# Kernel tuning notes

Measured on AMD Instinct MI355X. Metric: run time of the kernel, lower is better.

The kernel has to match this reference:

```python
import jax, jax.numpy as jnp
import numpy as np

N = 50000      # nodes
E = 800000     # edges (avg degree 16)
IN_DIM = 128
HIDDEN = 128
HEADS = 4
OUT = HIDDEN // HEADS  # 32 per-head out dim
NEG_SLOPE = 0.2        # DGL GATConv default leaky_relu slope


def setup_inputs() -> dict:
    key = jax.random.key(0)
    ks = jax.random.split(key, 12)
    x = jax.random.normal(ks[0], (N, IN_DIM), dtype=jnp.float32)
    src = jax.random.randint(ks[1], (E,), 0, N)
    dst = jax.random.randint(ks[2], (E,), 0, N)
    s = 0.1
    # layer 1 params
    W1 = jax.random.normal(ks[3], (IN_DIM, HEADS * OUT), dtype=jnp.float32) * s
    al1 = jax.random.normal(ks[4], (HEADS, OUT), dtype=jnp.float32) * s
    ar1 = jax.random.normal(ks[5], (HEADS, OUT), dtype=jnp.float32) * s
    b1 = jnp.zeros((HEADS * OUT,), dtype=jnp.float32)
    # layer 2 params (input = flattened heads of layer 1 = HIDDEN)
    W2 = jax.random.normal(ks[6], (HIDDEN, HEADS * OUT), dtype=jnp.float32) * s
    al2 = jax.random.normal(ks[7], (HEADS, OUT), dtype=jnp.float32) * s
    ar2 = jax.random.normal(ks[8], (HEADS, OUT), dtype=jnp.float32) * s
    b2 = jnp.zeros((HEADS * OUT,), dtype=jnp.float32)
    return {"x": x, "W1": W1, "al1": al1, "ar1": ar1, "b1": b1,
            "W2": W2, "al2": al2, "ar2": ar2, "b2": b2,
            "src": src, "dst": dst}


def gat_layer(x, W, a_l, a_r, b, src, dst):
    # x: [N, in], W: [in, H*D], a_l/a_r: [H, D], b: [H*D]
    z = (x @ W).reshape(N, HEADS, OUT)                # [N,H,D]
    el = jnp.sum(z * a_l[None], axis=-1)              # [N,H]
    er = jnp.sum(z * a_r[None], axis=-1)              # [N,H]
    e = jax.nn.leaky_relu(el[src] + er[dst], NEG_SLOPE)  # [E,H]
    # segment softmax over incoming edges of each dst node
    m = jax.ops.segment_max(e, dst, num_segments=N)   # [N,H]
    ex = jnp.exp(e - m[dst])                          # [E,H]
    s = jax.ops.segment_sum(ex, dst, num_segments=N)  # [N,H]
    alpha = ex / s[dst]                               # [E,H]
    out = jax.ops.segment_sum(z[src] * alpha[:, :, None], dst, num_segments=N)
    return out + b.reshape(1, HEADS, OUT)             # [N,H,D]


def reference(x, W1, al1, ar1, b1, W2, al2, ar2, b2, src, dst):
    # dropout is eval-mode (identity)
    h = gat_layer(x, W1, al1, ar1, b1, src, dst)      # [N,H,D]
    h = jax.nn.relu(h).reshape(N, HIDDEN)             # flatten heads between layers
    out = gat_layer(h, W2, al2, ar2, b2, src, dst)    # [N,H,D]
    return out
```

## Files before the change

### kernel.cpp

```cpp
#include <hip/hip_runtime.h>
#include <hip/hip_bf16.h>
#include <math.h>

#define N_NODES 50000
#define N_EDGES 800000
#define DIM 128
#define HEADS 4
#define CAP 64
#define NEG_SLOPE 0.2f
#define GEMM_BLKS 782
#define NBUCK 782
#define CAPB 1280
#define P1_BLKS 400
#define P1_EPB 2000

typedef __attribute__((ext_vector_type(8))) short bf16x8;
typedef __attribute__((ext_vector_type(4))) float f32x4;

__device__ __forceinline__ short f2bf_rne(float x) {
    __hip_bfloat16 h = __float2bfloat16(x);
    return *(short*)&h;
}
__device__ __forceinline__ float lrelu(float v) {
    return v > 0.f ? v : NEG_SLOPE * v;
}
__device__ __forceinline__ float blo(int z) { return __int_as_float(z << 16); }
__device__ __forceinline__ float bhi(int z) { return __int_as_float(z & 0xFFFF0000); }

__global__ __launch_bounds__(256) void prep_kernel(
    const float* __restrict__ W1, const float* __restrict__ W2,
    short* __restrict__ Wth, short* __restrict__ Wtl, int* __restrict__ gcur) {
    int t = blockIdx.x * blockDim.x + threadIdx.x;
    if (t < 2 * DIM * DIM) {
        int lay = t >> 14;
        int k = (t >> 7) & 127;
        int n = t & 127;
        float w = (lay ? W2 : W1)[k * DIM + n];
        int bits = __float_as_int(w);
        short hi = (short)(bits >> 16);
        float hif = __int_as_float(bits & 0xFFFF0000);
        Wth[lay * DIM * DIM + n * DIM + k] = hi;
        Wtl[lay * DIM * DIM + n * DIM + k] = f2bf_rne(w - hif);
    }
    if (t < NBUCK) gcur[t] = 0;
}

__device__ __forceinline__ void gemm_eler_body(
    int blk, int tid,
    const float* __restrict__ X, const short* __restrict__ Wth,
    const short* __restrict__ Wtl, const float* __restrict__ al,
    const float* __restrict__ ar, short* __restrict__ Zb,
    float* __restrict__ el, float* __restrict__ er, int nrows) {
    int wv = tid >> 6, lane = tid & 63;
    int row0 = blk * 64 + wv * 16;
    int c = lane & 15;
    int g = lane >> 4;
    int rA = row0 + c;
    int rAc = rA < nrows ? rA : nrows - 1;
    int koff = g * 8;

    f32x4 acc[8];
#pragma unroll
    for (int n = 0; n < 8; ++n) acc[n] = (f32x4){0.f, 0.f, 0.f, 0.f};

#pragma unroll
    for (int ks = 0; ks < 4; ++ks) {
        int k0 = ks * 32 + koff;
        float4 xa = *(const float4*)&X[(size_t)rAc * DIM + k0];
        float4 xb = *(const float4*)&X[(size_t)rAc * DIM + k0 + 4];
        float xs[8] = {xa.x, xa.y, xa.z, xa.w, xb.x, xb.y, xb.z, xb.w};
        bf16x8 ah, alo;
#pragma unroll
        for (int j = 0; j < 8; ++j) {
            int bits = __float_as_int(xs[j]);
            ah[j] = (short)(bits >> 16);
            float hif = __int_as_float(bits & 0xFFFF0000);
            alo[j] = f2bf_rne(xs[j] - hif);
        }
#pragma unroll
        for (int n = 0; n < 8; ++n) {
            int ncol = n * 16 + c;
            bf16x8 bh = *(const bf16x8*)&Wth[ncol * DIM + k0];
            bf16x8 bl = *(const bf16x8*)&Wtl[ncol * DIM + k0];
            acc[n] = __builtin_amdgcn_mfma_f32_16x16x32_bf16(ah, bh, acc[n], 0, 0, 0);
            acc[n] = __builtin_amdgcn_mfma_f32_16x16x32_bf16(alo, bh, acc[n], 0, 0, 0);
            acc[n] = __builtin_amdgcn_mfma_f32_16x16x32_bf16(ah, bl, acc[n], 0, 0, 0);
        }
    }

    int rb = row0 + g * 4;
#pragma unroll
    for (int n = 0; n < 8; ++n) {
#pragma unroll
        for (int r = 0; r < 4; ++r) {
            int row = rb + r;
            if (row < nrows)
                Zb[(size_t)row * DIM + n * 16 + c] = f2bf_rne(acc[n][r]);
        }
    }

    f32x4 elv[4], erv[4];
#pragma unroll
    for (int r = 0; r < 4; ++r) { elv[r] = (f32x4){0,0,0,0}; erv[r] = (f32x4){0,0,0,0}; }
#pragma unroll
    for (int n = 0; n < 8; ++n) {
        int h = n >> 1;
        int idx = ((n & 1) << 4) + c;
        float av = al[h * 32 + idx];
        float bv = ar[h * 32 + idx];
#pragma unroll
        for (int r = 0; r < 4; ++r) {
            elv[r][h] += acc[n][r] * av;
            erv[r][h] += acc[n][r] * bv;
        }
    }
#pragma unroll
    for (int m = 1; m <= 8; m <<= 1) {
#pragma unroll
        for (int r = 0; r < 4; ++r) {
#pragma unroll
            for (int h = 0; h < 4; ++h) {
                elv[r][h] += __shfl_xor(elv[r][h], m);
                erv[r][h] += __shfl_xor(erv[r][h], m);
            }
        }
    }
    if (c < 4) {
        int row = rb + c;
        if (row < nrows) {
            f32x4 eo = c == 0 ? elv[0] : c == 1 ? elv[1] : c == 2 ? elv[2] : elv[3];
            f32x4 ro = c == 0 ? erv[0] : c == 1 ? erv[1] : c == 2 ? erv[2] : erv[3];
            *(float4*)&el[row * 4] = make_float4(eo[0], eo[1], eo[2], eo[3]);
            *(float4*)&er[row * 4] = make_float4(ro[0], ro[1], ro[2], ro[3]);
        }
    }
}

__global__ __launch_bounds__(256) void fused_gemm_pass1_kernel(
    const float* __restrict__ X, const short* __restrict__ Wth,
    const short* __restrict__ Wtl, const float* __restrict__ al,
    const float* __restrict__ ar, short* __restrict__ Zb,
    float* __restrict__ el, float* __restrict__ er,
    const int* __restrict__ src, const int* __restrict__ dst,
    int* __restrict__ gcur, int2* __restrict__ pairs) {
    if (blockIdx.x < GEMM_BLKS) {
        gemm_eler_body(blockIdx.x, threadIdx.x, X, Wth, Wtl, al, ar, Zb, el, er, N_NODES);
        return;
    }
    __shared__ int hist[NBUCK], base_s[NBUCK], cur[NBUCK];
    int tid = threadIdx.x;
    for (int b = tid; b < NBUCK; b += 256) { hist[b] = 0; cur[b] = 0; }
    __syncthreads();
    int blk = blockIdx.x - GEMM_BLKS;
    int e0 = blk * P1_EPB;
    int e1 = e0 + P1_EPB; if (e1 > N_EDGES) e1 = N_EDGES;
    for (int i = e0 + tid; i < e1; i += 256)
        atomicAdd(&hist[dst[i] >> 6], 1);
    __syncthreads();
    for (int b = tid; b < NBUCK; b += 256)
        if (hist[b]) base_s[b] = atomicAdd(&gcur[b], hist[b]);
    __syncthreads();
    for (int i = e0 + tid; i < e1; i += 256) {
        int d = dst[i];
        int b = d >> 6;
        int pos = base_s[b] + atomicAdd(&cur[b], 1);
        if (pos < CAPB) pairs[b * CAPB + pos] = make_int2(src[i], d);
    }
}

#define GATHER_LOOP(FROW, STG, D, AX, AY, SM)                                   \
    {                                                                           \
        int j = 0;                                                              \
        for (; j + 8 <= (D); j += 8) {                                          \
            int4 sA = *(const int4*)&FROW[j];                                   \
            int4 sB = *(const int4*)&FROW[j + 4];                               \
            float4 pA = *(const float4*)&STG[j];                                \
            float4 pB = *(const float4*)&STG[j + 4];                            \
            int z0 = *(const int*)(zbase + ((size_t)sA.x << 8));                \
            int z1 = *(const int*)(zbase + ((size_t)sA.y << 8));                \
            int z2 = *(const int*)(zbase + ((size_t)sA.z << 8));                \
            int z3 = *(const int*)(zbase + ((size_t)sA.w << 8));                \
            int z4 = *(const int*)(zbase + ((size_t)sB.x << 8));                \
            int z5 = *(const int*)(zbase + ((size_t)sB.y << 8));                \
            int z6 = *(const int*)(zbase + ((size_t)sB.z << 8));                \
            int z7 = *(const int*)(zbase + ((size_t)sB.w << 8));                \
            AX += pA.x * blo(z0); AY += pA.x * bhi(z0);                         \
            AX += pA.y * blo(z1); AY += pA.y * bhi(z1);                         \
            AX += pA.z * blo(z2); AY += pA.z * bhi(z2);                         \
            AX += pA.w * blo(z3); AY += pA.w * bhi(z3);                         \
            AX += pB.x * blo(z4); AY += pB.x * bhi(z4);                         \
            AX += pB.y * blo(z5); AY += pB.y * bhi(z5);                         \
            AX += pB.z * blo(z6); AY += pB.z * bhi(z6);                         \
            AX += pB.w * blo(z7); AY += pB.w * bhi(z7);                         \
            SM += (pA.x + pA.y) + (pA.z + pA.w) + (pB.x + pB.y) + (pB.z + pB.w);\
        }                                                                       \
        for (; j + 4 <= (D); j += 4) {                                          \
            int4 sA = *(const int4*)&FROW[j];                                   \
            float4 pA = *(const float4*)&STG[j];                                \
            int z0 = *(const int*)(zbase + ((size_t)sA.x << 8));                \
            int z1 = *(const int*)(zbase + ((size_t)sA.y << 8));                \
            int z2 = *(const int*)(zbase + ((size_t)sA.z << 8));                \
            int z3 = *(const int*)(zbase + ((size_t)sA.w << 8));                \
            AX += pA.x * blo(z0); AY += pA.x * bhi(z0);                         \
            AX += pA.y * blo(z1); AY += pA.y * bhi(z1);                         \
            AX += pA.z * blo(z2); AY += pA.z * bhi(z2);                         \
            AX += pA.w * blo(z3); AY += pA.w * bhi(z3);                         \
            SM += (pA.x + pA.y) + (pA.z + pA.w);                                \
        }                                                                       \
        for (; j < (D); ++j) {                                                  \
            int s = FROW[j];                                                    \
            float pv = STG[j];                                                  \
            int zz = *(const int*)(zbase + ((size_t)s << 8));                   \
            AX += pv * blo(zz); AY += pv * bhi(zz);                             \
            SM += pv;                                                           \
        }                                                                       \
    }

__global__ __launch_bounds__(256) void gat1_gemm2_kernel(
    const int* __restrict__ gcur, const int2* __restrict__ pairs,
    const short* __restrict__ Zb1, const float* __restrict__ el1,
    const float* __restrict__ er1, const float* __restrict__ b1,
    const short* __restrict__ Wth2, const short* __restrict__ Wtl2,
    const float* __restrict__ al2, const float* __restrict__ ar2,
    short* __restrict__ Zb2, float* __restrict__ el2, float* __restrict__ er2) {
    __shared__ int fine[16][68];
    __shared__ int lcnt[16];
    __shared__ float stage[4][4][64];
    __shared__ unsigned int hh[16][68];
    int tid = threadIdx.x;
    int bkt = blockIdx.x >> 2;
    int q = blockIdx.x & 3;
    int nbase = (bkt << 6) + (q << 4);
    if (tid < 16) lcnt[tid] = 0;
    __syncthreads();
    int ne = gcur[bkt]; if (ne > CAPB) ne = CAPB;
    const int2* pb = pairs + (size_t)bkt * CAPB;
    for (int i = tid; i < ne; i += 256) {
        int2 p = pb[i];
        int ln = p.y & 63;
        if ((ln >> 4) == q) {
            int pos = atomicAdd(&lcnt[ln & 15], 1);
            if (pos < CAP) fine[ln & 15][pos] = p.x;
        }
    }
    __syncthreads();

    int wv = tid >> 6, lane = tid & 63, h = lane >> 4;
    const char* zbase = (const char*)Zb1 + lane * 4;
    float2 bb = *(const float2*)&b1[lane * 2];
#pragma unroll
    for (int u = 0; u < 4; ++u) {
        int n = (wv << 2) + u;
        int node = nbase + n;
        int d = lcnt[n]; d = d > CAP ? CAP : d;

        float p0 = 0.f, p1 = 0.f, p2 = 0.f, p3 = 0.f;
        if (lane < d) {
            int s = fine[n][lane];
            float4 er4 = *(const float4*)&er1[node * HEADS];
            float4 e4 = *(const float4*)&el1[s * HEADS];
            p0 = __expf(lrelu(e4.x + er4.x));
            p1 = __expf(lrelu(e4.y + er4.y));
            p2 = __expf(lrelu(e4.z + er4.z));
            p3 = __expf(lrelu(e4.w + er4.w));
        }
        stage[wv][0][lane] = p0;
        stage[wv][1][lane] = p1;
        stage[wv][2][lane] = p2;
        stage[wv][3][lane] = p3;

        float ax = 0.f, ay = 0.f, sm = 0.f;
        const int* frow = &fine[n][0];
        const float* stg = &stage[wv][h][0];
        GATHER_LOOP(frow, stg, d, ax, ay, sm)

        float inv = sm > 0.f ? 1.f / sm : 0.f;
        float ox = fmaxf(ax * inv + bb.x, 0.f);
        float oy = fmaxf(ay * inv + bb.y, 0.f);
        hh[n][lane] = (unsigned int)(unsigned short)f2bf_rne(ox) |
                      ((unsigned int)(unsigned short)f2bf_rne(oy) << 16);
    }
    __syncthreads();

    int c = lane & 15, g = lane >> 4;
    f32x4 acc[2];
    acc[0] = (f32x4){0.f, 0.f, 0.f, 0.f};
    acc[1] = (f32x4){0.f, 0.f, 0.f, 0.f};
#pragma unroll
    for (int ks = 0; ks < 4; ++ks) {
        int k0 = ks * 32 + g * 8;
        bf16x8 ah = *(const bf16x8*)((const short*)&hh[c][0] + k0);
#pragma unroll
        for (int n2 = 0; n2 < 2; ++n2) {
            int ncol = wv * 32 + n2 * 16 + c;
            bf16x8 bh = *(const bf16x8*)&Wth2[ncol * DIM + k0];
            bf16x8 bl = *(const bf16x8*)&Wtl2[ncol * DIM + k0];
            acc[n2] = __builtin_amdgcn_mfma_f32_16x16x32_bf16(ah, bh, acc[n2], 0, 0, 0);
            acc[n2] = __builtin_amdgcn_mfma_f32_16x16x32_bf16(ah, bl, acc[n2], 0, 0, 0);
        }
    }
    int rb = nbase + g * 4;
#pragma unroll
    for (int n2 = 0; n2 < 2; ++n2) {
#pragma unroll
        for (int r = 0; r < 4; ++r) {
            int row = rb + r;
            if (row < N_NODES)
                Zb2[(size_t)row * DIM + wv * 32 + n2 * 16 + c] = f2bf_rne(acc[n2][r]);
        }
    }
    float elv0 = 0.f, elv1 = 0.f, elv2 = 0.f, elv3 = 0.f;
    float erv0 = 0.f, erv1 = 0.f, erv2 = 0.f, erv3 = 0.f;
#pragma unroll
    for (int n2 = 0; n2 < 2; ++n2) {
        float av = al2[wv * 32 + n2 * 16 + c];
        float bv = ar2[wv * 32 + n2 * 16 + c];
        elv0 += acc[n2][0] * av; erv0 += acc[n2][0] * bv;
        elv1 += acc[n2][1] * av; erv1 += acc[n2][1] * bv;
        elv2 += acc[n2][2] * av; erv2 += acc[n2][2] * bv;
        elv3 += acc[n2][3] * av; erv3 += acc[n2][3] * bv;
    }
#pragma unroll
    for (int m = 1; m <= 8; m <<= 1) {
        elv0 += __shfl_xor(elv0, m); erv0 += __shfl_xor(erv0, m);
        elv1 += __shfl_xor(elv1, m); erv1 += __shfl_xor(erv1, m);
        elv2 += __shfl_xor(elv2, m); erv2 += __shfl_xor(erv2, m);
        elv3 += __shfl_xor(elv3, m); erv3 += __shfl_xor(erv3, m);
    }
    if (c < 4) {
        int row = rb + c;
        if (row < N_NODES) {
            float eo = c == 0 ? elv0 : c == 1 ? elv1 : c == 2 ? elv2 : elv3;
            float ro = c == 0 ? erv0 : c == 1 ? erv1 : c == 2 ? erv2 : erv3;
            el2[row * HEADS + wv] = eo;
            er2[row * HEADS + wv] = ro;
        }
    }
}

__global__ __launch_bounds__(256) void gat2_kernel(
    const int* __restrict__ gcur, const int2* __restrict__ pairs,
    const short* __restrict__ Zb2, const float* __restrict__ el2,
    const float* __restrict__ er2, const float* __restrict__ b2,
    float* __restrict__ out) {
    __shared__ int fine[16][68];
    __shared__ int lcnt[16];
    __shared__ float stage[4][4][64];
    int tid = threadIdx.x;
    int bkt = blockIdx.x >> 2;
    int q = blockIdx.x & 3;
    int nbase = (bkt << 6) + (q << 4);
    if (tid < 16) lcnt[tid] = 0;
    __syncthreads();
    int ne = gcur[bkt]; if (ne > CAPB) ne = CAPB;
    const int2* pb = pairs + (size_t)bkt * CAPB;
    for (int i = tid; i < ne; i += 256) {
        int2 p = pb[i];
        int ln = p.y & 63;
        if ((ln >> 4) == q) {
            int pos = atomicAdd(&lcnt[ln & 15], 1);
            if (pos < CAP) fine[ln & 15][pos] = p.x;
        }
    }
    __syncthreads();

    int wv = tid >> 6, lane = tid & 63, h = lane >> 4;
    const char* zbase = (const char*)Zb2 + lane * 4;
    float2 bb = *(const float2*)&b2[lane * 2];
#pragma unroll
    for (int u = 0; u < 4; ++u) {
        int n = (wv << 2) + u;
        int node = nbase + n;
        int d = lcnt[n]; d = d > CAP ? CAP : d;

        float p0 = 0.f, p1 = 0.f, p2 = 0.f, p3 = 0.f;
        if (lane < d) {
            int s = fine[n][lane];
            float4 er4 = *(const float4*)&er2[node * HEADS];
            float4 e4 = *(const float4*)&el2[s * HEADS];
            p0 = __expf(lrelu(e4.x + er4.x));
            p1 = __expf(lrelu(e4.y + er4.y));
            p2 = __expf(lrelu(e4.z + er4.z));
            p3 = __expf(lrelu(e4.w + er4.w));
        }
        stage[wv][0][lane] = p0;
        stage[wv][1][lane] = p1;
        stage[wv][2][lane] = p2;
        stage[wv][3][lane] = p3;

        float ax = 0.f, ay = 0.f, sm = 0.f;
        const int* frow = &fine[n][0];
        const float* stg = &stage[wv][h][0];
        GATHER_LOOP(frow, stg, d, ax, ay, sm)

        if (node < N_NODES) {
            float inv = sm > 0.f ? 1.f / sm : 0.f;
            float ox = ax * inv + bb.x;
            float oy = ay * inv + bb.y;
            *(float2*)&out[(size_t)node * DIM + lane * 2] = make_float2(ox, oy);
        }
    }
}

extern "C" void kernel_launch(void* const* d_in, const int* in_sizes, int n_in,
                              void* d_out, int out_size, void* d_ws, size_t ws_size,
                              hipStream_t stream) {
    const float* x   = (const float*)d_in[0];
    const float* W1  = (const float*)d_in[1];
    const float* al1 = (const float*)d_in[2];
    const float* ar1 = (const float*)d_in[3];
    const float* b1  = (const float*)d_in[4];
    const float* W2  = (const float*)d_in[5];
    const float* al2 = (const float*)d_in[6];
    const float* ar2 = (const float*)d_in[7];
    const float* b2  = (const float*)d_in[8];
    const int* src   = (const int*)d_in[9];
    const int* dst   = (const int*)d_in[10];

    char* ws = (char*)d_ws;
    short* Zb1  = (short*)ws; ws += (size_t)N_NODES * DIM * sizeof(short);
    short* Zb2  = (short*)ws; ws += (size_t)N_NODES * DIM * sizeof(short);
    float* el1  = (float*)ws; ws += (size_t)N_NODES * HEADS * sizeof(float);
    float* er1  = (float*)ws; ws += (size_t)N_NODES * HEADS * sizeof(float);
    float* el2  = (float*)ws; ws += (size_t)N_NODES * HEADS * sizeof(float);
    float* er2  = (float*)ws; ws += (size_t)N_NODES * HEADS * sizeof(float);
    int2*  pairs = (int2*)ws; ws += (size_t)NBUCK * CAPB * sizeof(int2);
    short* Wth  = (short*)ws; ws += (size_t)2 * DIM * DIM * sizeof(short);
    short* Wtl  = (short*)ws; ws += (size_t)2 * DIM * DIM * sizeof(short);
    int*   gcur = (int*)ws;   ws += (size_t)NBUCK * sizeof(int);

    const int BLK = 256;
    int grid_gat = NBUCK * 4;

    prep_kernel<<<128, BLK, 0, stream>>>(W1, W2, Wth, Wtl, gcur);
    fused_gemm_pass1_kernel<<<GEMM_BLKS + P1_BLKS, BLK, 0, stream>>>(
        x, Wth, Wtl, al1, ar1, Zb1, el1, er1, src, dst, gcur, pairs);
    gat1_gemm2_kernel<<<grid_gat, BLK, 0, stream>>>(
        gcur, pairs, Zb1, el1, er1, b1,
        Wth + DIM * DIM, Wtl + DIM * DIM, al2, ar2, Zb2, el2, er2);
    gat2_kernel<<<grid_gat, BLK, 0, stream>>>(gcur, pairs, Zb2, el2, er2, b2,
                                              (float*)d_out);
}
```

Before: 144.1 us.

## Stage gathered neighbor feature rows in shared memory with cooperative 16-byte loads

Replaces the per-lane 4-byte scattered gathers of bf16 Z rows with a block-cooperative scheme. In chunks of eight neighbors, each thread pair copies a full 256-byte source row into shared memory using int4 loads. All four waves then accumulate from LDS, with the attention weights precomputed for all 16 nodes in a shared buffer. The aim is wider memory transactions and more loads in flight. In exchange it adds two block barriers per chunk, iterates to the block's maximum degree (idle lanes on low-degree nodes), and uses more shared memory, which may reduce occupancy.

```diff
diff --git a/kernel.cpp b/kernel.cpp
--- a/kernel.cpp
+++ b/kernel.cpp
@@ -168,54 +168,6 @@
     }
 }
 
-#define GATHER_LOOP(FROW, STG, D, AX, AY, SM)                                   \
-    {                                                                           \
-        int j = 0;                                                              \
-        for (; j + 8 <= (D); j += 8) {                                          \
-            int4 sA = *(const int4*)&FROW[j];                                   \
-            int4 sB = *(const int4*)&FROW[j + 4];                               \
-            float4 pA = *(const float4*)&STG[j];                                \
-            float4 pB = *(const float4*)&STG[j + 4];                            \
-            int z0 = *(const int*)(zbase + ((size_t)sA.x << 8));                \
-            int z1 = *(const int*)(zbase + ((size_t)sA.y << 8));                \
-            int z2 = *(const int*)(zbase + ((size_t)sA.z << 8));                \
-            int z3 = *(const int*)(zbase + ((size_t)sA.w << 8));                \
-            int z4 = *(const int*)(zbase + ((size_t)sB.x << 8));                \
-            int z5 = *(const int*)(zbase + ((size_t)sB.y << 8));                \
-            int z6 = *(const int*)(zbase + ((size_t)sB.z << 8));                \
-            int z7 = *(const int*)(zbase + ((size_t)sB.w << 8));                \
-            AX += pA.x * blo(z0); AY += pA.x * bhi(z0);                         \
-            AX += pA.y * blo(z1); AY += pA.y * bhi(z1);                         \
-            AX += pA.z * blo(z2); AY += pA.z * bhi(z2);                         \
-            AX += pA.w * blo(z3); AY += pA.w * bhi(z3);                         \
-            AX += pB.x * blo(z4); AY += pB.x * bhi(z4);                         \
-            AX += pB.y * blo(z5); AY += pB.y * bhi(z5);                         \
-            AX += pB.z * blo(z6); AY += pB.z * bhi(z6);                         \
-            AX += pB.w * blo(z7); AY += pB.w * bhi(z7);                         \
-            SM += (pA.x + pA.y) + (pA.z + pA.w) + (pB.x + pB.y) + (pB.z + pB.w);\
-        }                                                                       \
-        for (; j + 4 <= (D); j += 4) {                                          \
-            int4 sA = *(const int4*)&FROW[j];                                   \
-            float4 pA = *(const float4*)&STG[j];                                \
-            int z0 = *(const int*)(zbase + ((size_t)sA.x << 8));                \
-            int z1 = *(const int*)(zbase + ((size_t)sA.y << 8));                \
-            int z2 = *(const int*)(zbase + ((size_t)sA.z << 8));                \
-            int z3 = *(const int*)(zbase + ((size_t)sA.w << 8));                \
-            AX += pA.x * blo(z0); AY += pA.x * bhi(z0);                         \
-            AX += pA.y * blo(z1); AY += pA.y * bhi(z1);                         \
-            AX += pA.z * blo(z2); AY += pA.z * bhi(z2);                         \
-            AX += pA.w * blo(z3); AY += pA.w * bhi(z3);                         \
-            SM += (pA.x + pA.y) + (pA.z + pA.w);                                \
-        }                                                                       \
-        for (; j < (D); ++j) {                                                  \
-            int s = FROW[j];                                                    \
-            float pv = STG[j];                                                  \
-            int zz = *(const int*)(zbase + ((size_t)s << 8));                   \
-            AX += pv * blo(zz); AY += pv * bhi(zz);                             \
-            SM += pv;                                                           \
-        }                                                                       \
-    }
-
 __global__ __launch_bounds__(256) void gat1_gemm2_kernel(
     const int* __restrict__ gcur, const int2* __restrict__ pairs,
     const short* __restrict__ Zb1, const float* __restrict__ el1,
@@ -225,8 +177,10 @@
     short* __restrict__ Zb2, float* __restrict__ el2, float* __restrict__ er2) {
     __shared__ int fine[16][68];
     __shared__ int lcnt[16];
-    __shared__ float stage[4][4][64];
+    __shared__ float pstage[16][4][68];
+    __shared__ short zs[16][8][136];
     __shared__ unsigned int hh[16][68];
+    __shared__ int maxd_s;
     int tid = threadIdx.x;
     int bkt = blockIdx.x >> 2;
     int q = blockIdx.x & 3;
@@ -246,14 +200,19 @@
     __syncthreads();
 
     int wv = tid >> 6, lane = tid & 63, h = lane >> 4;
-    const char* zbase = (const char*)Zb1 + lane * 4;
-    float2 bb = *(const float2*)&b1[lane * 2];
+    if (tid == 0) {
+        int m = 0;
+#pragma unroll
+        for (int i = 0; i < 16; ++i) { int dd = lcnt[i]; if (dd > m) m = dd; }
+        maxd_s = m > CAP ? CAP : m;
+    }
+    int dloc[4];
 #pragma unroll
     for (int u = 0; u < 4; ++u) {
         int n = (wv << 2) + u;
         int node = nbase + n;
         int d = lcnt[n]; d = d > CAP ? CAP : d;
-
+        dloc[u] = d;
         float p0 = 0.f, p1 = 0.f, p2 = 0.f, p3 = 0.f;
         if (lane < d) {
             int s = fine[n][lane];
@@ -264,19 +223,54 @@
             p2 = __expf(lrelu(e4.z + er4.z));
             p3 = __expf(lrelu(e4.w + er4.w));
         }
-        stage[wv][0][lane] = p0;
-        stage[wv][1][lane] = p1;
-        stage[wv][2][lane] = p2;
-        stage[wv][3][lane] = p3;
-
-        float ax = 0.f, ay = 0.f, sm = 0.f;
-        const int* frow = &fine[n][0];
-        const float* stg = &stage[wv][h][0];
-        GATHER_LOOP(frow, stg, d, ax, ay, sm)
-
-        float inv = sm > 0.f ? 1.f / sm : 0.f;
-        float ox = fmaxf(ax * inv + bb.x, 0.f);
-        float oy = fmaxf(ay * inv + bb.y, 0.f);
+        pstage[n][0][lane] = p0;
+        pstage[n][1][lane] = p1;
+        pstage[n][2][lane] = p2;
+        pstage[n][3][lane] = p3;
+    }
+    __syncthreads();
+
+    float ax[4] = {0.f, 0.f, 0.f, 0.f};
+    float ay[4] = {0.f, 0.f, 0.f, 0.f};
+    float sm[4] = {0.f, 0.f, 0.f, 0.f};
+    int maxd = maxd_s;
+    int gs = tid >> 1, ghr = tid & 1;
+    int gn = gs >> 3, gjj = gs & 7;
+    int gd = lcnt[gn]; gd = gd > CAP ? CAP : gd;
+    for (int jc = 0; jc < maxd; jc += 8) {
+        int j = jc + gjj;
+        if (j < gd) {
+            int srcn = fine[gn][j];
+            const int4* gp = (const int4*)((const char*)Zb1 + ((size_t)srcn << 8) + (ghr << 7));
+            int4* dp = (int4*)&zs[gn][gjj][ghr * 64];
+#pragma unroll
+            for (int k = 0; k < 8; ++k) dp[k] = gp[k];
+        }
+        __syncthreads();
+#pragma unroll
+        for (int u = 0; u < 4; ++u) {
+            int n = (wv << 2) + u;
+            int rem = dloc[u] - jc;
+            rem = rem > 8 ? 8 : rem;
+            const float* pst = &pstage[n][h][jc];
+            for (int jj = 0; jj < rem; ++jj) {
+                float pv = pst[jj];
+                int zz = *(const int*)&zs[n][jj][lane * 2];
+                ax[u] += pv * blo(zz);
+                ay[u] += pv * bhi(zz);
+                sm[u] += pv;
+            }
+        }
+        __syncthreads();
+    }
+
+    float2 bb = *(const float2*)&b1[lane * 2];
+#pragma unroll
+    for (int u = 0; u < 4; ++u) {
+        int n = (wv << 2) + u;
+        float inv = sm[u] > 0.f ? 1.f / sm[u] : 0.f;
+        float ox = fmaxf(ax[u] * inv + bb.x, 0.f);
+        float oy = fmaxf(ay[u] * inv + bb.y, 0.f);
         hh[n][lane] = (unsigned int)(unsigned short)f2bf_rne(ox) |
                       ((unsigned int)(unsigned short)f2bf_rne(oy) << 16);
     }
@@ -345,7 +339,9 @@
     float* __restrict__ out) {
     __shared__ int fine[16][68];
     __shared__ int lcnt[16];
-    __shared__ float stage[4][4][64];
+    __shared__ float pstage[16][4][68];
+    __shared__ short zs[16][8][136];
+    __shared__ int maxd_s;
     int tid = threadIdx.x;
     int bkt = blockIdx.x >> 2;
     int q = blockIdx.x & 3;
@@ -365,14 +361,19 @@
     __syncthreads();
 
     int wv = tid >> 6, lane = tid & 63, h = lane >> 4;
-    const char* zbase = (const char*)Zb2 + lane * 4;
-    float2 bb = *(const float2*)&b2[lane * 2];
+    if (tid == 0) {
+        int m = 0;
+#pragma unroll
+        for (int i = 0; i < 16; ++i) { int dd = lcnt[i]; if (dd > m) m = dd; }
+        maxd_s = m > CAP ? CAP : m;
+    }
+    int dloc[4];
 #pragma unroll
     for (int u = 0; u < 4; ++u) {
         int n = (wv << 2) + u;
         int node = nbase + n;
         int d = lcnt[n]; d = d > CAP ? CAP : d;
-
+        dloc[u] = d;
         float p0 = 0.f, p1 = 0.f, p2 = 0.f, p3 = 0.f;
         if (lane < d) {
             int s = fine[n][lane];
@@ -383,20 +384,56 @@
             p2 = __expf(lrelu(e4.z + er4.z));
             p3 = __expf(lrelu(e4.w + er4.w));
         }
-        stage[wv][0][lane] = p0;
-        stage[wv][1][lane] = p1;
-        stage[wv][2][lane] = p2;
-        stage[wv][3][lane] = p3;
-
-        float ax = 0.f, ay = 0.f, sm = 0.f;
-        const int* frow = &fine[n][0];
-        const float* stg = &stage[wv][h][0];
-        GATHER_LOOP(frow, stg, d, ax, ay, sm)
-
+        pstage[n][0][lane] = p0;
+        pstage[n][1][lane] = p1;
+        pstage[n][2][lane] = p2;
+        pstage[n][3][lane] = p3;
+    }
+    __syncthreads();
+
+    float ax[4] = {0.f, 0.f, 0.f, 0.f};
+    float ay[4] = {0.f, 0.f, 0.f, 0.f};
+    float sm[4] = {0.f, 0.f, 0.f, 0.f};
+    int maxd = maxd_s;
+    int gs = tid >> 1, ghr = tid & 1;
+    int gn = gs >> 3, gjj = gs & 7;
+    int gd = lcnt[gn]; gd = gd > CAP ? CAP : gd;
+    for (int jc = 0; jc < maxd; jc += 8) {
+        int j = jc + gjj;
+        if (j < gd) {
+            int srcn = fine[gn][j];
+            const int4* gp = (const int4*)((const char*)Zb2 + ((size_t)srcn << 8) + (ghr << 7));
+            int4* dp = (int4*)&zs[gn][gjj][ghr * 64];
+#pragma unroll
+            for (int k = 0; k < 8; ++k) dp[k] = gp[k];
+        }
+        __syncthreads();
+#pragma unroll
+        for (int u = 0; u < 4; ++u) {
+            int n = (wv << 2) + u;
+            int rem = dloc[u] - jc;
+            rem = rem > 8 ? 8 : rem;
+            const float* pst = &pstage[n][h][jc];
+            for (int jj = 0; jj < rem; ++jj) {
+                float pv = pst[jj];
+                int zz = *(const int*)&zs[n][jj][lane * 2];
+                ax[u] += pv * blo(zz);
+                ay[u] += pv * bhi(zz);
+                sm[u] += pv;
+            }
+        }
+        __syncthreads();
+    }
+
+    float2 bb = *(const float2*)&b2[lane * 2];
+#pragma unroll
+    for (int u = 0; u < 4; ++u) {
+        int n = (wv << 2) + u;
+        int node = nbase + n;
         if (node < N_NODES) {
-            float inv = sm > 0.f ? 1.f / sm : 0.f;
-            float ox = ax * inv + bb.x;
-            float oy = ay * inv + bb.y;
+            float inv = sm[u] > 0.f ? 1.f / sm[u] : 0.f;
+            float ox = ax[u] * inv + bb.x;
+            float oy = ay[u] * inv + bb.y;
             *(float2*)&out[(size_t)node * DIM + lane * 2] = make_float2(ox, oy);
         }
     }
```

After: 248.8 us. 72.7% more time.
